# Optimization experiments

Hardware: AMD Instinct MI355X
Metric: run time of the kernel (lower is better)

The kernel has to match this reference:

```python
import jax, jax.numpy as jnp
import numpy as np

EPS = 1e-10


def setup_inputs() -> dict:
    key = jax.random.key(0)
    ks = jax.random.split(key, 8)
    b, s, m, r, n = 2, 2048, 1024, 64, 16
    u = jax.random.normal(ks[0], (b, s, m), dtype=jnp.float32)
    delta = jax.random.normal(ks[1], (b, s, r), dtype=jnp.float32)
    dt_proj_w = jax.random.normal(ks[2], (m, r), dtype=jnp.float32) * 0.02
    dt_proj_b = jax.random.normal(ks[3], (m,), dtype=jnp.float32) * 0.02
    # A_log ~ Uniform(-3, -1) as in nn.init.uniform_(self.A_log, -3.0, -1.0)
    A_log = jax.random.uniform(ks[4], (n, m), dtype=jnp.float32, minval=-3.0, maxval=-1.0)
    D_skip = jnp.ones((m,), dtype=jnp.float32)
    # xavier_uniform with gain=0.1 on [n, m]
    bound = 0.1 * np.sqrt(6.0 / (n + m))
    B_proj_w = jax.random.uniform(ks[5], (n, m), dtype=jnp.float32, minval=-bound, maxval=bound)
    C_proj_w = jax.random.uniform(ks[6], (n, m), dtype=jnp.float32, minval=-bound, maxval=bound)
    return {"u": u, "delta": delta, "dt_proj_w": dt_proj_w, "dt_proj_b": dt_proj_b,
            "A_log": A_log, "D_skip": D_skip, "B_proj_w": B_proj_w, "C_proj_w": C_proj_w}


def reference(u, delta, dt_proj_w, dt_proj_b, A_log, D_skip, B_proj_w, C_proj_w):
    # u: [b, s, m]; delta: [b, s, r]
    dt = jax.nn.softplus(jnp.einsum('bsr,mr->bsm', delta, dt_proj_w) + dt_proj_b)
    dt = jnp.clip(dt, 1e-6, 10.0)                      # [b, s, m]
    A = jnp.clip(-jnp.exp(A_log), -10.0, -1e-6)        # [n, m]
    B = jnp.einsum('bsm,nm->bsn', u, B_proj_w)         # [b, s, n]
    C = jnp.einsum('bsm,nm->bsn', u, C_proj_w)         # [b, s, n]

    # associative-scan path (seq_len > 256), math as in _associative_scan:
    # h_t = exp(cumsum_t log(dA)) * cumsum_t (dB_u / dA)
    dA = jnp.exp(dt[:, :, None, :] * A[None, None])    # [b, s, n, m]
    dA_c = jnp.clip(dA, EPS, None)
    dBu = dt[:, :, None, :] * B[..., None] * u[:, :, None, :]  # [b, s, n, m]
    A_cum = jnp.exp(jnp.cumsum(jnp.log(dA_c), axis=1))
    h = A_cum * jnp.cumsum(dBu / dA_c, axis=1)          # [b, s, n, m]
    y = jnp.einsum('bsnm,bsn->bsm', h, C)               # contract state dim

    out = y + u * D_skip
    out = jnp.clip(out, -10000.0, 10000.0)
    bad = jnp.any(~jnp.isfinite(out))
    return jnp.where(bad, jnp.zeros_like(u), out)
```

## Files before the change

kernel.cpp:

```cpp
#include <hip/hip_runtime.h>
#include <hip/hip_bf16.h>
#include <math.h>

#define B_ 2
#define S_ 2048
#define M_ 1024
#define R_ 64
#define N_ 16
#define NC 64
#define CH (S_/NC)

#define DT_OFF  0
#define P_OFF   4194304
#define H_OFF   6291456
#define BP_OFF  8388608
#define CP_OFF  8454144
#define BWT_OFF 8519680
#define CWT_OFF 8536064
#define PB_OFF  8552448
#define PC_OFF  8814592

__global__ __launch_bounds__(256) void k_prep(const float* __restrict__ Bw,
                                              const float* __restrict__ Cw,
                                              float* __restrict__ BwT,
                                              float* __restrict__ CwT) {
    int idx = blockIdx.x * 256 + threadIdx.x;
    int m = idx >> 4, n = idx & 15;
    BwT[idx] = Bw[n * M_ + m];
    CwT[idx] = Cw[n * M_ + m];
}

__global__ __launch_bounds__(256) void k_dt(const float* __restrict__ delta,
                                            const float* __restrict__ Wdt,
                                            const float* __restrict__ bdt,
                                            float* __restrict__ dt) {
    int m    = blockIdx.x * 256 + threadIdx.x;
    int row0 = blockIdx.y * 8;
    float w[R_];
    const float4* W4 = reinterpret_cast<const float4*>(Wdt + (size_t)m * R_);
#pragma unroll
    for (int i = 0; i < R_ / 4; ++i) {
        float4 v = W4[i];
        w[4*i] = v.x; w[4*i+1] = v.y; w[4*i+2] = v.z; w[4*i+3] = v.w;
    }
    float bias = bdt[m];
#pragma unroll 1
    for (int r = 0; r < 8; ++r) {
        int bs = row0 + r;
        const float* dr = delta + (size_t)bs * R_;
        float acc = bias;
#pragma unroll
        for (int k = 0; k < R_; ++k) acc = fmaf(dr[k], w[k], acc);
        float sp = fmaxf(acc, 0.f) + log1pf(expf(-fabsf(acc)));
        sp = fminf(fmaxf(sp, 1e-6f), 10.0f);
        dt[(size_t)bs * M_ + m] = sp;
    }
}

__global__ __launch_bounds__(256) void k_bc_partial(const float* __restrict__ u,
                                                    const float* __restrict__ BwT,
                                                    const float* __restrict__ CwT,
                                                    float* __restrict__ pB,
                                                    float* __restrict__ pC) {
    __shared__ float uLds[16 * 260];
    int r0 = blockIdx.x * 16;
    int k0 = blockIdx.y * 256;
    for (int i = threadIdx.x; i < 4096; i += 256) {
        int r = i >> 8, k = i & 255;
        uLds[r * 260 + k] = u[(size_t)(r0 + r) * M_ + k0 + k];
    }
    __syncthreads();
    int r = threadIdx.x >> 4, n = threadIdx.x & 15;
    const float4* u4 = reinterpret_cast<const float4*>(uLds + r * 260);
    float accB = 0.f, accC = 0.f;
#pragma unroll 4
    for (int k4 = 0; k4 < 64; ++k4) {
        float4 uv = u4[k4];
        int kb = k0 + k4 * 4;
        accB = fmaf(uv.x, BwT[(kb+0)*16 + n], accB);
        accB = fmaf(uv.y, BwT[(kb+1)*16 + n], accB);
        accB = fmaf(uv.z, BwT[(kb+2)*16 + n], accB);
        accB = fmaf(uv.w, BwT[(kb+3)*16 + n], accB);
        accC = fmaf(uv.x, CwT[(kb+0)*16 + n], accC);
        accC = fmaf(uv.y, CwT[(kb+1)*16 + n], accC);
        accC = fmaf(uv.z, CwT[(kb+2)*16 + n], accC);
        accC = fmaf(uv.w, CwT[(kb+3)*16 + n], accC);
    }
    size_t o = (size_t)blockIdx.y * 65536 + (size_t)(r0 + r) * 16 + n;
    pB[o] = accB;
    pC[o] = accC;
}

__global__ __launch_bounds__(256) void k_bc_reduce(const float* __restrict__ pB,
                                                   const float* __restrict__ pC,
                                                   float* __restrict__ Bp,
                                                   float* __restrict__ Cp) {
    int idx = blockIdx.x * 256 + threadIdx.x;
    float sB = 0.f, sC = 0.f;
#pragma unroll
    for (int ks = 0; ks < 4; ++ks) {
        sB += pB[(size_t)ks * 65536 + idx];
        sC += pC[(size_t)ks * 65536 + idx];
    }
    Bp[idx] = sB;
    Cp[idx] = sC;
}

__global__ __launch_bounds__(256) void k_pass1(const float* __restrict__ dt,
                                               const float* __restrict__ u,
                                               const float* __restrict__ Bp,
                                               const float* __restrict__ A_log,
                                               float* __restrict__ P,
                                               float* __restrict__ H) {
    __shared__ float ldsDt[CH * 64], ldsU[CH * 64], ldsB[CH * 16];
    int m0 = blockIdx.x * 64, c = blockIdx.y, b = blockIdx.z;
    int s0 = c * CH;
    int tid = threadIdx.x;
    for (int i = tid; i < CH * 64; i += 256) {
        int s = i >> 6, ml = i & 63;
        size_t off = ((size_t)(b * S_ + s0 + s)) * M_ + m0 + ml;
        ldsDt[i] = dt[off];
        ldsU[i]  = u[off];
    }
    for (int i = tid; i < CH * 16; i += 256)
        ldsB[i] = Bp[(size_t)(b * S_ + s0) * N_ + i];
    __syncthreads();
    int lane = tid & 63, wave = tid >> 6;
    int ml = wave * 16 + (lane & 15);
    int m  = m0 + ml;
    int n0 = (lane >> 4) * 4;
    float Aa[4], h[4] = {0,0,0,0}, g[4] = {1.f,1.f,1.f,1.f};
#pragma unroll
    for (int j = 0; j < 4; ++j) {
        float a = -expf(A_log[(size_t)(n0 + j) * M_ + m]);
        Aa[j] = fminf(fmaxf(a, -10.f), -1e-6f);
    }
    for (int s = 0; s < CH; ++s) {
        float dtv = ldsDt[s * 64 + ml];
        float uv  = ldsU [s * 64 + ml];
        float du  = dtv * uv;
        float4 bv = *reinterpret_cast<const float4*>(&ldsB[s * 16 + n0]);
        float bb[4] = {bv.x, bv.y, bv.z, bv.w};
#pragma unroll
        for (int j = 0; j < 4; ++j) {
            float ea = __expf(dtv * Aa[j]);
            h[j] = fmaf(ea, h[j], g[j] * (du * bb[j]));
            g[j] *= ea;
        }
    }
#pragma unroll
    for (int j = 0; j < 4; ++j) {
        size_t o = ((size_t)(b * 16 + n0 + j) * NC + c) * M_ + m;
        P[o] = g[j];
        H[o] = h[j];
    }
}

__global__ __launch_bounds__(256) void k_pass2(float* __restrict__ P,
                                               float* __restrict__ H) {
    int idx = blockIdx.x * 256 + threadIdx.x;
    int m = idx & (M_ - 1);
    int n = (idx >> 10) & 15;
    int b = idx >> 14;
    size_t base = ((size_t)(b * 16 + n) * NC) * M_ + m;
    float grun = 1.f, hrun = 0.f;
#pragma unroll 1
    for (int c0 = 0; c0 < NC; c0 += 8) {
        float pv[8], hv[8];
#pragma unroll
        for (int t = 0; t < 8; ++t) {
            pv[t] = P[base + (size_t)(c0 + t) * M_];
            hv[t] = H[base + (size_t)(c0 + t) * M_];
        }
#pragma unroll
        for (int t = 0; t < 8; ++t) {
            P[base + (size_t)(c0 + t) * M_] = grun;
            H[base + (size_t)(c0 + t) * M_] = hrun;
            hrun = fmaf(pv[t], hrun, grun * hv[t]);
            grun *= pv[t];
        }
    }
}

__global__ __launch_bounds__(256) void k_pass3(const float* __restrict__ dt,
                                               const float* __restrict__ u,
                                               const float* __restrict__ Bp,
                                               const float* __restrict__ Cp,
                                               const float* __restrict__ A_log,
                                               const float* __restrict__ Dskip,
                                               const float* __restrict__ Pinit,
                                               const float* __restrict__ Hinit,
                                               float* __restrict__ out) {
    __shared__ float ldsDt[CH * 64], ldsU[CH * 64], ldsB[CH * 16], ldsC[CH * 16];
    int m0 = blockIdx.x * 64, c = blockIdx.y, b = blockIdx.z;
    int s0 = c * CH;
    int tid = threadIdx.x;
    for (int i = tid; i < CH * 64; i += 256) {
        int s = i >> 6, ml = i & 63;
        size_t off = ((size_t)(b * S_ + s0 + s)) * M_ + m0 + ml;
        ldsDt[i] = dt[off];
        ldsU[i]  = u[off];
    }
    for (int i = tid; i < CH * 16; i += 256) {
        ldsB[i] = Bp[(size_t)(b * S_ + s0) * N_ + i];
        ldsC[i] = Cp[(size_t)(b * S_ + s0) * N_ + i];
    }
    __syncthreads();
    int lane = tid & 63, wave = tid >> 6;
    int ml = wave * 16 + (lane & 15);
    int m  = m0 + ml;
    int ng = lane >> 4, n0 = ng * 4;
    float Aa[4], h[4], g[4];
#pragma unroll
    for (int j = 0; j < 4; ++j) {
        float a = -expf(A_log[(size_t)(n0 + j) * M_ + m]);
        Aa[j] = fminf(fmaxf(a, -10.f), -1e-6f);
        size_t o = ((size_t)(b * 16 + n0 + j) * NC + c) * M_ + m;
        g[j] = Pinit[o];
        h[j] = Hinit[o];
    }
    float Dm = Dskip[m];
    for (int s = 0; s < CH; ++s) {
        float dtv = ldsDt[s * 64 + ml];
        float uv  = ldsU [s * 64 + ml];
        float du  = dtv * uv;
        float4 bv = *reinterpret_cast<const float4*>(&ldsB[s * 16 + n0]);
        float4 cv = *reinterpret_cast<const float4*>(&ldsC[s * 16 + n0]);
        float bb[4] = {bv.x, bv.y, bv.z, bv.w};
        float cc[4] = {cv.x, cv.y, cv.z, cv.w};
        float y = 0.f;
#pragma unroll
        for (int j = 0; j < 4; ++j) {
            float ea = __expf(dtv * Aa[j]);
            h[j] = fmaf(ea, h[j], g[j] * (du * bb[j]));
            g[j] *= ea;
            y = fmaf(h[j], cc[j], y);
        }
        y += __shfl_xor(y, 16, 64);
        y += __shfl_xor(y, 32, 64);
        if (ng == 0) {
            float o = y + uv * Dm;
            o = fminf(fmaxf(o, -10000.f), 10000.f);
            out[((size_t)(b * S_ + s0 + s)) * M_ + m] = o;
        }
    }
}

extern "C" void kernel_launch(void* const* d_in, const int* in_sizes, int n_in,
                              void* d_out, int out_size, void* d_ws, size_t ws_size,
                              hipStream_t stream) {
    const float* u     = (const float*)d_in[0];
    const float* delta = (const float*)d_in[1];
    const float* Wdt   = (const float*)d_in[2];
    const float* bdt   = (const float*)d_in[3];
    const float* A_log = (const float*)d_in[4];
    const float* Dski  = (const float*)d_in[5];
    const float* Bw    = (const float*)d_in[6];
    const float* Cw    = (const float*)d_in[7];
    float* out = (float*)d_out;
    float* ws  = (float*)d_ws;

    float* dt  = ws + DT_OFF;
    float* P   = ws + P_OFF;
    float* H   = ws + H_OFF;
    float* Bp  = ws + BP_OFF;
    float* Cp  = ws + CP_OFF;
    float* BwT = ws + BWT_OFF;
    float* CwT = ws + CWT_OFF;
    float* pB  = ws + PB_OFF;
    float* pC  = ws + PC_OFF;

    k_prep<<<64, 256, 0, stream>>>(Bw, Cw, BwT, CwT);
    k_dt<<<dim3(4, 512), 256, 0, stream>>>(delta, Wdt, bdt, dt);
    k_bc_partial<<<dim3(256, 4), 256, 0, stream>>>(u, BwT, CwT, pB, pC);
    k_bc_reduce<<<256, 256, 0, stream>>>(pB, pC, Bp, Cp);
    k_pass1<<<dim3(16, NC, B_), 256, 0, stream>>>(dt, u, Bp, A_log, P, H);
    k_pass2<<<128, 256, 0, stream>>>(P, H);
    k_pass3<<<dim3(16, NC, B_), 256, 0, stream>>>(dt, u, Bp, Cp, A_log, Dski, P, H, out);
}
```

Baseline: 114.7 us.

## Fuse prep and B/C reduce into neighbours, vectorize loads, widen pass2 grid

The transpose of the B/C projection weights moves into the dt kernel, and the separate B/C partial-sum reduce kernel is removed. The K split drops from four to two, and pass1 and pass3 now add the two partials while loading. The staging loads in the B/C projection and both scan passes use float4, and pass2 launches 512 blocks of 64 threads instead of 128 blocks of 256. This removes two kernel launches and their global round trips, and spreads the serial chunk-combine scan over more workgroups. The cost is longer per-block reductions in the projection and a little redundant partial summing in pass1 and pass3.

```diff
diff --git a/kernel.cpp b/kernel.cpp
--- a/kernel.cpp
+++ b/kernel.cpp
@@ -13,27 +13,26 @@
 #define DT_OFF  0
 #define P_OFF   4194304
 #define H_OFF   6291456
-#define BP_OFF  8388608
-#define CP_OFF  8454144
-#define BWT_OFF 8519680
-#define CWT_OFF 8536064
-#define PB_OFF  8552448
-#define PC_OFF  8814592
-
-__global__ __launch_bounds__(256) void k_prep(const float* __restrict__ Bw,
-                                              const float* __restrict__ Cw,
-                                              float* __restrict__ BwT,
-                                              float* __restrict__ CwT) {
-    int idx = blockIdx.x * 256 + threadIdx.x;
-    int m = idx >> 4, n = idx & 15;
-    BwT[idx] = Bw[n * M_ + m];
-    CwT[idx] = Cw[n * M_ + m];
-}
+#define BWT_OFF 8388608
+#define CWT_OFF 8404992
+#define PB_OFF  8421376
+#define PC_OFF  8552448
 
 __global__ __launch_bounds__(256) void k_dt(const float* __restrict__ delta,
                                             const float* __restrict__ Wdt,
                                             const float* __restrict__ bdt,
-                                            float* __restrict__ dt) {
+                                            const float* __restrict__ Bw,
+                                            const float* __restrict__ Cw,
+                                            float* __restrict__ dt,
+                                            float* __restrict__ BwT,
+                                            float* __restrict__ CwT) {
+    int bid = blockIdx.y * 4 + blockIdx.x;
+    if (threadIdx.x < 8) {
+        int idx = bid * 8 + threadIdx.x;
+        int mt = idx >> 4, nt = idx & 15;
+        BwT[idx] = Bw[nt * M_ + mt];
+        CwT[idx] = Cw[nt * M_ + mt];
+    }
     int m    = blockIdx.x * 256 + threadIdx.x;
     int row0 = blockIdx.y * 8;
     float w[R_];
@@ -62,19 +61,20 @@
                                                     const float* __restrict__ CwT,
                                                     float* __restrict__ pB,
                                                     float* __restrict__ pC) {
-    __shared__ float uLds[16 * 260];
+    __shared__ float uLds[16 * 516];
     int r0 = blockIdx.x * 16;
-    int k0 = blockIdx.y * 256;
-    for (int i = threadIdx.x; i < 4096; i += 256) {
-        int r = i >> 8, k = i & 255;
-        uLds[r * 260 + k] = u[(size_t)(r0 + r) * M_ + k0 + k];
+    int k0 = blockIdx.y * 512;
+    for (int i = threadIdx.x; i < 2048; i += 256) {
+        int r = i >> 7, kq = i & 127;
+        float4 v = *reinterpret_cast<const float4*>(&u[(size_t)(r0 + r) * M_ + k0 + kq * 4]);
+        *reinterpret_cast<float4*>(&uLds[r * 516 + kq * 4]) = v;
     }
     __syncthreads();
     int r = threadIdx.x >> 4, n = threadIdx.x & 15;
-    const float4* u4 = reinterpret_cast<const float4*>(uLds + r * 260);
+    const float4* u4 = reinterpret_cast<const float4*>(uLds + r * 516);
     float accB = 0.f, accC = 0.f;
 #pragma unroll 4
-    for (int k4 = 0; k4 < 64; ++k4) {
+    for (int k4 = 0; k4 < 128; ++k4) {
         float4 uv = u4[k4];
         int kb = k0 + k4 * 4;
         accB = fmaf(uv.x, BwT[(kb+0)*16 + n], accB);
@@ -91,24 +91,9 @@
     pC[o] = accC;
 }
 
-__global__ __launch_bounds__(256) void k_bc_reduce(const float* __restrict__ pB,
-                                                   const float* __restrict__ pC,
-                                                   float* __restrict__ Bp,
-                                                   float* __restrict__ Cp) {
-    int idx = blockIdx.x * 256 + threadIdx.x;
-    float sB = 0.f, sC = 0.f;
-#pragma unroll
-    for (int ks = 0; ks < 4; ++ks) {
-        sB += pB[(size_t)ks * 65536 + idx];
-        sC += pC[(size_t)ks * 65536 + idx];
-    }
-    Bp[idx] = sB;
-    Cp[idx] = sC;
-}
-
 __global__ __launch_bounds__(256) void k_pass1(const float* __restrict__ dt,
                                                const float* __restrict__ u,
-                                               const float* __restrict__ Bp,
+                                               const float* __restrict__ pB,
                                                const float* __restrict__ A_log,
                                                float* __restrict__ P,
                                                float* __restrict__ H) {
@@ -116,14 +101,17 @@
     int m0 = blockIdx.x * 64, c = blockIdx.y, b = blockIdx.z;
     int s0 = c * CH;
     int tid = threadIdx.x;
-    for (int i = tid; i < CH * 64; i += 256) {
-        int s = i >> 6, ml = i & 63;
-        size_t off = ((size_t)(b * S_ + s0 + s)) * M_ + m0 + ml;
-        ldsDt[i] = dt[off];
-        ldsU[i]  = u[off];
-    }
-    for (int i = tid; i < CH * 16; i += 256)
-        ldsB[i] = Bp[(size_t)(b * S_ + s0) * N_ + i];
+    for (int i = tid; i < 512; i += 256) {
+        int s = i >> 4, mq = (i & 15) * 4;
+        size_t off = ((size_t)(b * S_ + s0 + s)) * M_ + m0 + mq;
+        *reinterpret_cast<float4*>(&ldsDt[s * 64 + mq]) = *reinterpret_cast<const float4*>(&dt[off]);
+        *reinterpret_cast<float4*>(&ldsU [s * 64 + mq]) = *reinterpret_cast<const float4*>(&u[off]);
+    }
+    {
+        size_t base = (size_t)(b * S_ + s0) * N_;
+        for (int i = tid; i < CH * 16; i += 256)
+            ldsB[i] = pB[base + i] + pB[65536 + base + i];
+    }
     __syncthreads();
     int lane = tid & 63, wave = tid >> 6;
     int ml = wave * 16 + (lane & 15);
@@ -156,9 +144,9 @@
     }
 }
 
-__global__ __launch_bounds__(256) void k_pass2(float* __restrict__ P,
-                                               float* __restrict__ H) {
-    int idx = blockIdx.x * 256 + threadIdx.x;
+__global__ __launch_bounds__(64) void k_pass2(float* __restrict__ P,
+                                              float* __restrict__ H) {
+    int idx = blockIdx.x * 64 + threadIdx.x;
     int m = idx & (M_ - 1);
     int n = (idx >> 10) & 15;
     int b = idx >> 14;
@@ -184,8 +172,8 @@
 
 __global__ __launch_bounds__(256) void k_pass3(const float* __restrict__ dt,
                                                const float* __restrict__ u,
-                                               const float* __restrict__ Bp,
-                                               const float* __restrict__ Cp,
+                                               const float* __restrict__ pB,
+                                               const float* __restrict__ pC,
                                                const float* __restrict__ A_log,
                                                const float* __restrict__ Dskip,
                                                const float* __restrict__ Pinit,
@@ -195,15 +183,18 @@
     int m0 = blockIdx.x * 64, c = blockIdx.y, b = blockIdx.z;
     int s0 = c * CH;
     int tid = threadIdx.x;
-    for (int i = tid; i < CH * 64; i += 256) {
-        int s = i >> 6, ml = i & 63;
-        size_t off = ((size_t)(b * S_ + s0 + s)) * M_ + m0 + ml;
-        ldsDt[i] = dt[off];
-        ldsU[i]  = u[off];
-    }
-    for (int i = tid; i < CH * 16; i += 256) {
-        ldsB[i] = Bp[(size_t)(b * S_ + s0) * N_ + i];
-        ldsC[i] = Cp[(size_t)(b * S_ + s0) * N_ + i];
+    for (int i = tid; i < 512; i += 256) {
+        int s = i >> 4, mq = (i & 15) * 4;
+        size_t off = ((size_t)(b * S_ + s0 + s)) * M_ + m0 + mq;
+        *reinterpret_cast<float4*>(&ldsDt[s * 64 + mq]) = *reinterpret_cast<const float4*>(&dt[off]);
+        *reinterpret_cast<float4*>(&ldsU [s * 64 + mq]) = *reinterpret_cast<const float4*>(&u[off]);
+    }
+    {
+        size_t base = (size_t)(b * S_ + s0) * N_;
+        for (int i = tid; i < CH * 16; i += 256) {
+            ldsB[i] = pB[base + i] + pB[65536 + base + i];
+            ldsC[i] = pC[base + i] + pC[65536 + base + i];
+        }
     }
     __syncthreads();
     int lane = tid & 63, wave = tid >> 6;
@@ -263,18 +254,14 @@
     float* dt  = ws + DT_OFF;
     float* P   = ws + P_OFF;
     float* H   = ws + H_OFF;
-    float* Bp  = ws + BP_OFF;
-    float* Cp  = ws + CP_OFF;
     float* BwT = ws + BWT_OFF;
     float* CwT = ws + CWT_OFF;
     float* pB  = ws + PB_OFF;
     float* pC  = ws + PC_OFF;
 
-    k_prep<<<64, 256, 0, stream>>>(Bw, Cw, BwT, CwT);
-    k_dt<<<dim3(4, 512), 256, 0, stream>>>(delta, Wdt, bdt, dt);
-    k_bc_partial<<<dim3(256, 4), 256, 0, stream>>>(u, BwT, CwT, pB, pC);
-    k_bc_reduce<<<256, 256, 0, stream>>>(pB, pC, Bp, Cp);
-    k_pass1<<<dim3(16, NC, B_), 256, 0, stream>>>(dt, u, Bp, A_log, P, H);
-    k_pass2<<<128, 256, 0, stream>>>(P, H);
-    k_pass3<<<dim3(16, NC, B_), 256, 0, stream>>>(dt, u, Bp, Cp, A_log, Dski, P, H, out);
-}
+    k_dt<<<dim3(4, 512), 256, 0, stream>>>(delta, Wdt, bdt, Bw, Cw, dt, BwT, CwT);
+    k_bc_partial<<<dim3(256, 2), 256, 0, stream>>>(u, BwT, CwT, pB, pC);
+    k_pass1<<<dim3(16, NC, B_), 256, 0, stream>>>(dt, u, pB, A_log, P, H);
+    k_pass2<<<512, 64, 0, stream>>>(P, H);
+    k_pass3<<<dim3(16, NC, B_), 256, 0, stream>>>(dt, u, pB, pC, A_log, Dski, P, H, out);
+}
```

New measurement: 106.8 us. -6.9%, faster.
